# Kernel tuning notes

Measured on AMD Instinct MI355X. Metric: run time of the kernel, lower is better.

Reference implementation:

```python
import jax, jax.numpy as jnp
import numpy as np

UNITS = 768
OUT_STEPS = 64
INPUT_DIM = 96


def setup_inputs() -> dict:
    key = jax.random.key(0)
    ks = jax.random.split(key, 7)
    B, T = 2048, 24
    s_ih = 1.0 / np.sqrt(UNITS)
    inputs = jax.random.normal(ks[0], (B, T, INPUT_DIM), dtype=jnp.float32)
    # PyTorch LSTMCell params: weight_ih [4U, I], weight_hh [4U, U], biases [4U]
    W_ih = jax.random.uniform(ks[1], (4 * UNITS, INPUT_DIM), minval=-s_ih, maxval=s_ih, dtype=jnp.float32)
    W_hh = jax.random.uniform(ks[2], (4 * UNITS, UNITS), minval=-s_ih, maxval=s_ih, dtype=jnp.float32)
    b_ih = jax.random.uniform(ks[3], (4 * UNITS,), minval=-s_ih, maxval=s_ih, dtype=jnp.float32)
    b_hh = jax.random.uniform(ks[4], (4 * UNITS,), minval=-s_ih, maxval=s_ih, dtype=jnp.float32)
    # Dense: Linear(units, input_dim)
    s_d = 1.0 / np.sqrt(UNITS)
    W_d = jax.random.uniform(ks[5], (INPUT_DIM, UNITS), minval=-s_d, maxval=s_d, dtype=jnp.float32)
    b_d = jax.random.uniform(ks[6], (INPUT_DIM,), minval=-s_d, maxval=s_d, dtype=jnp.float32)
    return {"inputs": inputs, "W_ih": W_ih, "W_hh": W_hh, "b_ih": b_ih, "b_hh": b_hh, "W_d": W_d, "b_d": b_d}


def _lstm_cell(x, h, c, W_ih, W_hh, b_ih, b_hh):
    # gates: [B, 4U], PyTorch gate order i, f, g, o
    gates = x @ W_ih.T + b_ih + h @ W_hh.T + b_hh
    i, f, g, o = jnp.split(gates, 4, axis=-1)
    i = jax.nn.sigmoid(i)
    f = jax.nn.sigmoid(f)
    g = jnp.tanh(g)
    o = jax.nn.sigmoid(o)
    c_new = f * c + i * g
    h_new = o * jnp.tanh(c_new)
    return h_new, c_new


def reference(inputs, W_ih, W_hh, b_ih, b_hh, W_d, b_d):
    B = inputs.shape[0]
    h0 = jnp.zeros((B, UNITS), dtype=inputs.dtype)
    c0 = jnp.zeros((B, UNITS), dtype=inputs.dtype)
    # warmup: feed last timestep
    x0 = inputs[:, -1, :]
    h, c = _lstm_cell(x0, h0, c0, W_ih, W_hh, b_ih, b_hh)
    pred0 = h @ W_d.T + b_d

    def step(carry, _):
        pred, h, c = carry
        h2, c2 = _lstm_cell(pred, h, c, W_ih, W_hh, b_ih, b_hh)
        pred2 = h2 @ W_d.T + b_d
        return (pred2, h2, c2), pred2

    _, preds_rest = jax.lax.scan(step, (pred0, h, c), None, length=OUT_STEPS - 1)
    # preds_rest: [out_steps-1, B, I] -> stack with pred0 along time axis 1
    preds = jnp.concatenate([pred0[None], preds_rest], axis=0)  # [out_steps, B, I]
    return jnp.transpose(preds, (1, 0, 2))  # [B, out_steps, I]
```

## Files before the change

kernel.cpp:

```cpp
#include <hip/hip_runtime.h>
#include <hip/hip_bf16.h>
#include <stdint.h>

typedef __hip_bfloat16 bf16_t;
typedef __attribute__((ext_vector_type(4))) float f32x4;
typedef __attribute__((ext_vector_type(8))) short s16x8;

#define UNITS 768
#define NCOLS 3072
#define NPRED 96
#define MROWS 2048
#define BM 128
#define BN 128
#define BK 32

#define WAIT_VMCNT8 0xF78

#define GLL16(ldsp, gp) \
  __builtin_amdgcn_global_load_lds((const __attribute__((address_space(1))) void*)(gp), \
                                   (__attribute__((address_space(3))) void*)(ldsp), 16, 0, 0)

__device__ __forceinline__ float sigf(float x) {
    return __builtin_amdgcn_rcpf(1.f + __expf(-x));
}
__device__ __forceinline__ float tanh_fast(float x) {
    return 1.f - 2.f * __builtin_amdgcn_rcpf(1.f + __expf(2.f * x));
}


__global__ void prep_b0(const float* __restrict__ W_ih, bf16_t* __restrict__ B0T) {
    int idx = blockIdx.x * 256 + threadIdx.x;
    if (idx >= NCOLS * 96) return;
    int c = idx / 96, k = idx % 96;
    int u = ((c >> 6) << 4) + (c & 15);
    int g = (c >> 4) & 3;
    B0T[idx] = (bf16_t)W_ih[(g * UNITS + u) * 96 + k];
}

__global__ void prep_x0(const float* __restrict__ inputs, bf16_t* __restrict__ x0) {
    int idx = blockIdx.x * 256 + threadIdx.x;
    int b = idx / 96, k = idx % 96;
    x0[idx] = (bf16_t)inputs[(b * 24 + 23) * 96 + k];
}

__global__ void prep_bias(const float* __restrict__ b_ih, const float* __restrict__ b_hh,
                          const float* __restrict__ W_ih, const float* __restrict__ b_d,
                          float* __restrict__ b0_r, float* __restrict__ beff_r) {
    int c = blockIdx.x * 256 + threadIdx.x;
    if (c >= NCOLS) return;
    int u = ((c >> 6) << 4) + (c & 15);
    int g = (c >> 4) & 3;
    int r = g * UNITS + u;
    float v = b_ih[r] + b_hh[r];
    float acc = 0.f;
    for (int j = 0; j < 96; ++j) acc += W_ih[r * 96 + j] * b_d[j];
    b0_r[c] = v;
    beff_r[c] = v + acc;
}

__global__ void prep_beff2(const float* __restrict__ W_hh, const float* __restrict__ W_ih,
                           const float* __restrict__ W_d, bf16_t* __restrict__ BeffT) {
    __shared__ float sWih[64][96];
    __shared__ float sWd[96][64];
    const int c0 = blockIdx.x * 64, k0 = blockIdx.y * 64;
    const int tid = threadIdx.x;
    for (int i = tid; i < 64 * 96; i += 256) {
        int cc = i / 96, j = i % 96;
        int c = c0 + cc;
        int u = ((c >> 6) << 4) + (c & 15);
        int g = (c >> 4) & 3;
        sWih[cc][j] = W_ih[(g * UNITS + u) * 96 + j];
    }
    for (int i = tid; i < 96 * 64; i += 256) {
        int j = i / 64, kk = i % 64;
        sWd[j][kk] = W_d[j * UNITS + k0 + kk];
    }
    __syncthreads();
    const int kk = tid & 63;
    const int cc0 = (tid >> 6) * 16;
    for (int cc = cc0; cc < cc0 + 16; ++cc) {
        float acc = 0.f;
#pragma unroll 12
        for (int j = 0; j < 96; ++j) acc += sWih[cc][j] * sWd[j][kk];
        int c = c0 + cc;
        int u = ((c >> 6) << 4) + (c & 15);
        int g = (c >> 4) & 3;
        int r = g * UNITS + u;
        BeffT[(size_t)c * UNITS + k0 + kk] = (bf16_t)(W_hh[(size_t)r * UNITS + k0 + kk] + acc);
    }
}

__global__ void prep_wdt(const float* __restrict__ W_d, bf16_t* __restrict__ BeffT) {
    int idx = blockIdx.x * 256 + threadIdx.x;
    int c = idx / UNITS, k = idx % UNITS;
    float v = (c < NPRED) ? W_d[c * UNITS + k] : 0.f;
    BeffT[(size_t)(NCOLS + c) * UNITS + k] = (bf16_t)v;
}

__global__ __launch_bounds__(256, 2)
void step_kernel(const bf16_t* __restrict__ A,
                 const bf16_t* __restrict__ BT,
                 const float* __restrict__ bias_r,
                 const float* __restrict__ b_d,
                 float* __restrict__ c_state,
                 bf16_t* __restrict__ h_out,
                 float* __restrict__ out,
                 int Kdim, int nt_off, int t, int is_first)
{
    __shared__ bf16_t sAll[4][2][BM * BK];

    const int tid = threadIdx.x;
    const int wave = tid >> 6;
    const int lane = tid & 63;
    const int wr = wave >> 1, wc = wave & 1;
    const int l15 = lane & 15, l4 = lane >> 4;

    const int per = gridDim.x >> 3;
    const int g = (blockIdx.x & 7) * per + (blockIdx.x >> 3);
    const int nt = nt_off + (g >> 4);
    const int mt = g & 15;
    const int m0 = mt * BM;
    const int n0 = nt * BN;
    const bool is_pred = (nt >= 24);

    const int u = nt * 32 + wc * 16 + l15;
    const int slot = nt * 16 + mt;
    float* cbase = c_state + (((size_t)slot * 4 + wave) * 64 + lane) * 16;
    f32x4 cold4[4];
    float bi[4];
#pragma unroll
    for (int q = 0; q < 4; ++q) cold4[q] = f32x4{0.f, 0.f, 0.f, 0.f};
    if (!is_pred) {
        if (!is_first) {
#pragma unroll
            for (int q = 0; q < 4; ++q) cold4[q] = *(const f32x4*)(cbase + q * 4);
        }
#pragma unroll
        for (int f = 0; f < 4; ++f) bi[f] = bias_r[n0 + wc * 64 + f * 16 + l15];
    } else {
#pragma unroll
        for (int f = 0; f < 4; ++f) {
            int j = wc * 64 + f * 16 + l15;
            bi[f] = (j < NPRED) ? b_d[j] : 0.f;
        }
    }
    asm volatile("" ::: "memory");

    f32x4 acc[4][4];
#pragma unroll
    for (int i = 0; i < 4; ++i)
#pragma unroll
        for (int j = 0; j < 4; ++j) acc[i][j] = f32x4{0.f, 0.f, 0.f, 0.f};

    const int o0 = wave * 1024 + lane * 16;
    const int nk = Kdim >> 5;

#define STAGE(BUF, KT) do {                                                         \
        const int _kt = ((KT) < nk) ? (KT) : (nk - 1);                              \
        const int _k0 = _kt << 5;                                                   \
        bf16_t* _dA = &sAll[(BUF)][0][0];                                           \
        bf16_t* _dB = &sAll[(BUF)][1][0];                                           \
        _Pragma("unroll")                                                           \
        for (int _r = 0; _r < 2; ++_r) {                                            \
            int _ob = o0 + _r * 4096;                                               \
            int _row = _ob >> 6;                                                    \
            int _kb = _ob & 63;                                                     \
            const bf16_t* _gA = A + (size_t)(m0 + _row) * Kdim + _k0 + (_kb >> 1);  \
            GLL16(_dA + ((wave * 1024 + _r * 4096) >> 1), _gA);                     \
            const bf16_t* _gB = BT + (size_t)(n0 + _row) * Kdim + _k0 + (_kb >> 1); \
            GLL16(_dB + ((wave * 1024 + _r * 4096) >> 1), _gB);                     \
        }                                                                           \
    } while (0)

    STAGE(0, 0);
    STAGE(1, 1);
    STAGE(2, 2);

    for (int kt = 0; kt < nk; ++kt) {
        __builtin_amdgcn_s_waitcnt(WAIT_VMCNT8);
        __builtin_amdgcn_s_barrier();
        asm volatile("" ::: "memory");

        const int cb = kt & 3;
        const char* sAc = (const char*)&sAll[cb][0][0];
        const char* sBc = (const char*)&sAll[cb][1][0];

        s16x8 af[4], bfr[4];
#pragma unroll
        for (int f = 0; f < 4; ++f) {
            af[f]  = *(const s16x8*)(sAc + (wr * 64 + f * 16 + l15) * 64 + l4 * 16);
            bfr[f] = *(const s16x8*)(sBc + (wc * 64 + f * 16 + l15) * 64 + l4 * 16);
        }

        STAGE((kt + 3) & 3, kt + 3);

#pragma unroll
        for (int i = 0; i < 4; ++i)
#pragma unroll
            for (int j = 0; j < 4; ++j)
                acc[i][j] = __builtin_amdgcn_mfma_f32_16x16x32_bf16(af[i], bfr[j], acc[i][j], 0, 0, 0);
    }
#undef STAGE

    if (!is_pred) {
        f32x4 cnew4[4];
#pragma unroll
        for (int i = 0; i < 4; ++i) {
#pragma unroll
            for (int r = 0; r < 4; ++r) {
                int row = m0 + wr * 64 + i * 16 + l4 * 4 + r;
                float gi = acc[i][0][r] + bi[0];
                float gf = acc[i][1][r] + bi[1];
                float gg = acc[i][2][r] + bi[2];
                float go = acc[i][3][r] + bi[3];
                float si = sigf(gi);
                float sf = sigf(gf);
                float tg = tanh_fast(gg);
                float so = sigf(go);
                float cn = sf * cold4[i][r] + si * tg;
                cnew4[i][r] = cn;
                h_out[(size_t)row * UNITS + u] = (bf16_t)(so * tanh_fast(cn));
            }
        }
#pragma unroll
        for (int q = 0; q < 4; ++q) *(f32x4*)(cbase + q * 4) = cnew4[q];
    } else {
#pragma unroll
        for (int f = 0; f < 4; ++f) {
            int j = wc * 64 + f * 16 + l15;
            if (j < NPRED) {
#pragma unroll
                for (int i = 0; i < 4; ++i)
#pragma unroll
                    for (int r = 0; r < 4; ++r) {
                        int row = m0 + wr * 64 + i * 16 + l4 * 4 + r;
                        out[((size_t)row * 64 + (t - 1)) * NPRED + j] = acc[i][f][r] + bi[f];
                    }
            }
        }
    }
}

extern "C" void kernel_launch(void* const* d_in, const int* in_sizes, int n_in,
                              void* d_out, int out_size, void* d_ws, size_t ws_size,
                              hipStream_t stream)
{
    const float* inputs = (const float*)d_in[0];
    const float* W_ih   = (const float*)d_in[1];
    const float* W_hh   = (const float*)d_in[2];
    const float* b_ih   = (const float*)d_in[3];
    const float* b_hh   = (const float*)d_in[4];
    const float* W_d    = (const float*)d_in[5];
    const float* b_d    = (const float*)d_in[6];
    float* out = (float*)d_out;

    char* ws = (char*)d_ws;
    size_t off = 0;
    auto alloc = [&](size_t bytes) -> char* {
        char* p = ws + off;
        off = (off + bytes + 255) & ~(size_t)255;
        return p;
    };
    bf16_t* B0T   = (bf16_t*)alloc((size_t)NCOLS * 96 * 2);
    bf16_t* BeffT = (bf16_t*)alloc((size_t)3200 * UNITS * 2);
    bf16_t* x0    = (bf16_t*)alloc((size_t)MROWS * 96 * 2);
    bf16_t* h0    = (bf16_t*)alloc((size_t)MROWS * UNITS * 2);
    bf16_t* h1    = (bf16_t*)alloc((size_t)MROWS * UNITS * 2);
    float*  cst   = (float*)alloc((size_t)MROWS * UNITS * 4);
    float*  b0r   = (float*)alloc(NCOLS * 4);
    float*  beffr = (float*)alloc(NCOLS * 4);

    prep_b0   <<<(NCOLS * 96 + 255) / 256, 256, 0, stream>>>(W_ih, B0T);
    prep_x0   <<<(MROWS * 96) / 256, 256, 0, stream>>>(inputs, x0);
    prep_bias <<<(NCOLS + 255) / 256, 256, 0, stream>>>(b_ih, b_hh, W_ih, b_d, b0r, beffr);
    prep_beff2<<<dim3(48, 12), 256, 0, stream>>>(W_hh, W_ih, W_d, BeffT);
    prep_wdt  <<<(128 * UNITS) / 256, 256, 0, stream>>>(W_d, BeffT);

    bf16_t* h[2] = {h0, h1};

    step_kernel<<<384, 256, 0, stream>>>(x0, B0T, b0r, b_d, cst, h[1], out, 96, 0, 0, 1);
    for (int n = 1; n < 64; ++n)
        step_kernel<<<400, 256, 0, stream>>>(h[n & 1], BeffT, beffr, b_d, cst,
                                             h[(n + 1) & 1], out, UNITS, 0, n, 0);
    step_kernel<<<16, 256, 0, stream>>>(h[0], BeffT, beffr, b_d, cst, h[1], out,
                                        UNITS, 24, 64, 0);
    (void)ws_size; (void)in_sizes; (void)n_in; (void)out_size;
}
```

Baseline: 1.407 ms.

## Pre-swizzle operands into MFMA fragment layout and load directly to registers

Weights and the hidden state are rearranged into a fragment-major layout, so each lane's 16-byte MFMA operand sits contiguously in global memory. The step kernel then drops LDS staging and barriers and loads A/B fragments straight into registers, using a 3-deep register ring. The LSTM epilogue writes h in the same swizzled layout so the next step can read it directly. This removes LDS traffic and block-wide synchronisation. In exchange it costs more VGPRs, loses the sharing of tiles across waves, so each wave fetches its own operands through L1/L2, and adds prep passes.

New measurement: 1.349 ms. 4.1% less time.

```diff
diff --git a/kernel.cpp b/kernel.cpp
--- a/kernel.cpp
+++ b/kernel.cpp
@@ -10,15 +10,6 @@
 #define NCOLS 3072
 #define NPRED 96
 #define MROWS 2048
-#define BM 128
-#define BN 128
-#define BK 32
-
-#define WAIT_VMCNT8 0xF78
-
-#define GLL16(ldsp, gp) \
-  __builtin_amdgcn_global_load_lds((const __attribute__((address_space(1))) void*)(gp), \
-                                   (__attribute__((address_space(3))) void*)(ldsp), 16, 0, 0)
 
 __device__ __forceinline__ float sigf(float x) {
     return __builtin_amdgcn_rcpf(1.f + __expf(-x));
@@ -39,8 +30,14 @@
 
 __global__ void prep_x0(const float* __restrict__ inputs, bf16_t* __restrict__ x0) {
     int idx = blockIdx.x * 256 + threadIdx.x;
-    int b = idx / 96, k = idx % 96;
-    x0[idx] = (bf16_t)inputs[(b * 24 + 23) * 96 + k];
+    int j = idx & 7;
+    int l = (idx >> 3) & 63;
+    int fg = idx >> 9;
+    int kf = fg % 3;
+    int mf = fg / 3;
+    int m = mf * 16 + (l & 15);
+    int k = kf * 32 + (l >> 4) * 8 + j;
+    x0[idx] = (bf16_t)inputs[(m * 24 + 23) * 96 + k];
 }
 
 __global__ void prep_bias(const float* __restrict__ b_ih, const float* __restrict__ b_hh,
@@ -97,18 +94,32 @@
     BeffT[(size_t)(NCOLS + c) * UNITS + k] = (bf16_t)v;
 }
 
+__global__ void prep_swz(const bf16_t* __restrict__ src, bf16_t* __restrict__ dst,
+                         int Knk, int K, int total) {
+    int idx = blockIdx.x * 256 + threadIdx.x;
+    if (idx >= total) return;
+    int j = idx & 7;
+    int l = (idx >> 3) & 63;
+    int fg = idx >> 9;
+    int f = fg & 3;
+    int rest = fg >> 2;
+    int kf = rest % Knk;
+    int nw = rest / Knk;
+    int c = (nw >> 1) * 128 + (nw & 1) * 64 + f * 16 + (l & 15);
+    int k = kf * 32 + (l >> 4) * 8 + j;
+    dst[idx] = src[(size_t)c * K + k];
+}
+
 __global__ __launch_bounds__(256, 2)
 void step_kernel(const bf16_t* __restrict__ A,
-                 const bf16_t* __restrict__ BT,
+                 const bf16_t* __restrict__ B,
                  const float* __restrict__ bias_r,
                  const float* __restrict__ b_d,
                  float* __restrict__ c_state,
                  bf16_t* __restrict__ h_out,
                  float* __restrict__ out,
-                 int Kdim, int nt_off, int t, int is_first)
+                 int Knk, int nt_off, int t, int is_first)
 {
-    __shared__ bf16_t sAll[4][2][BM * BK];
-
     const int tid = threadIdx.x;
     const int wave = tid >> 6;
     const int lane = tid & 63;
@@ -119,9 +130,17 @@
     const int g = (blockIdx.x & 7) * per + (blockIdx.x >> 3);
     const int nt = nt_off + (g >> 4);
     const int mt = g & 15;
-    const int m0 = mt * BM;
-    const int n0 = nt * BN;
+    const int n0 = nt * 128;
     const bool is_pred = (nt >= 24);
+
+    const bf16_t* Ab[4];
+#pragma unroll
+    for (int i = 0; i < 4; ++i)
+        Ab[i] = A + ((size_t)((mt * 8 + wr * 4 + i) * Knk) * 64 + lane) * 8;
+    const bf16_t* Bb[4];
+#pragma unroll
+    for (int f = 0; f < 4; ++f)
+        Bb[f] = B + ((size_t)((nt * 2 + wc) * Knk * 4 + f) * 64 + lane) * 8;
 
     const int u = nt * 32 + wc * 16 + l15;
     const int slot = nt * 16 + mt;
@@ -144,7 +163,6 @@
             bi[f] = (j < NPRED) ? b_d[j] : 0.f;
         }
     }
-    asm volatile("" ::: "memory");
 
     f32x4 acc[4][4];
 #pragma unroll
@@ -152,63 +170,51 @@
 #pragma unroll
         for (int j = 0; j < 4; ++j) acc[i][j] = f32x4{0.f, 0.f, 0.f, 0.f};
 
-    const int o0 = wave * 1024 + lane * 16;
-    const int nk = Kdim >> 5;
-
-#define STAGE(BUF, KT) do {                                                         \
-        const int _kt = ((KT) < nk) ? (KT) : (nk - 1);                              \
-        const int _k0 = _kt << 5;                                                   \
-        bf16_t* _dA = &sAll[(BUF)][0][0];                                           \
-        bf16_t* _dB = &sAll[(BUF)][1][0];                                           \
-        _Pragma("unroll")                                                           \
-        for (int _r = 0; _r < 2; ++_r) {                                            \
-            int _ob = o0 + _r * 4096;                                               \
-            int _row = _ob >> 6;                                                    \
-            int _kb = _ob & 63;                                                     \
-            const bf16_t* _gA = A + (size_t)(m0 + _row) * Kdim + _k0 + (_kb >> 1);  \
-            GLL16(_dA + ((wave * 1024 + _r * 4096) >> 1), _gA);                     \
-            const bf16_t* _gB = BT + (size_t)(n0 + _row) * Kdim + _k0 + (_kb >> 1); \
-            GLL16(_dB + ((wave * 1024 + _r * 4096) >> 1), _gB);                     \
-        }                                                                           \
+    s16x8 afr[3][4], bfr[3][4];
+    const int nk = Knk;
+
+#define LOADK(BUF, KT) do {                                                          \
+        _Pragma("unroll")                                                            \
+        for (int _i = 0; _i < 4; ++_i)                                               \
+            afr[BUF][_i] = *(const s16x8*)(Ab[_i] + (size_t)(KT) * 512);             \
+        _Pragma("unroll")                                                            \
+        for (int _f = 0; _f < 4; ++_f)                                               \
+            bfr[BUF][_f] = *(const s16x8*)(Bb[_f] + (size_t)(KT) * 2048);            \
     } while (0)
-
-    STAGE(0, 0);
-    STAGE(1, 1);
-    STAGE(2, 2);
-
-    for (int kt = 0; kt < nk; ++kt) {
-        __builtin_amdgcn_s_waitcnt(WAIT_VMCNT8);
-        __builtin_amdgcn_s_barrier();
-        asm volatile("" ::: "memory");
-
-        const int cb = kt & 3;
-        const char* sAc = (const char*)&sAll[cb][0][0];
-        const char* sBc = (const char*)&sAll[cb][1][0];
-
-        s16x8 af[4], bfr[4];
-#pragma unroll
-        for (int f = 0; f < 4; ++f) {
-            af[f]  = *(const s16x8*)(sAc + (wr * 64 + f * 16 + l15) * 64 + l4 * 16);
-            bfr[f] = *(const s16x8*)(sBc + (wc * 64 + f * 16 + l15) * 64 + l4 * 16);
-        }
-
-        STAGE((kt + 3) & 3, kt + 3);
-
-#pragma unroll
-        for (int i = 0; i < 4; ++i)
-#pragma unroll
-            for (int j = 0; j < 4; ++j)
-                acc[i][j] = __builtin_amdgcn_mfma_f32_16x16x32_bf16(af[i], bfr[j], acc[i][j], 0, 0, 0);
-    }
-#undef STAGE
+#define MF(BUF) do {                                                                 \
+        _Pragma("unroll")                                                            \
+        for (int _i = 0; _i < 4; ++_i)                                               \
+            _Pragma("unroll")                                                        \
+            for (int _j = 0; _j < 4; ++_j)                                           \
+                acc[_i][_j] = __builtin_amdgcn_mfma_f32_16x16x32_bf16(               \
+                    afr[BUF][_i], bfr[BUF][_j], acc[_i][_j], 0, 0, 0);               \
+    } while (0)
+
+    LOADK(0, 0);
+    LOADK(1, 1);
+    const int nk3 = nk / 3;
+    for (int b3 = 0; b3 < nk3; ++b3) {
+        const int kt = b3 * 3;
+        if (kt + 2 < nk) LOADK(2, kt + 2);
+        MF(0);
+        if (kt + 3 < nk) LOADK(0, kt + 3);
+        MF(1);
+        if (kt + 4 < nk) LOADK(1, kt + 4);
+        MF(2);
+    }
+#undef LOADK
+#undef MF
 
     if (!is_pred) {
+        const int kq = wc * 2 + (l15 >> 3);
+        const int jj = l15 & 7;
         f32x4 cnew4[4];
 #pragma unroll
         for (int i = 0; i < 4; ++i) {
+            const int mf = mt * 8 + wr * 4 + i;
+            bf16_t* hb = h_out + (size_t)(mf * 24 + nt) * 512;
 #pragma unroll
             for (int r = 0; r < 4; ++r) {
-                int row = m0 + wr * 64 + i * 16 + l4 * 4 + r;
                 float gi = acc[i][0][r] + bi[0];
                 float gf = acc[i][1][r] + bi[1];
                 float gg = acc[i][2][r] + bi[2];
@@ -219,7 +225,8 @@
                 float so = sigf(go);
                 float cn = sf * cold4[i][r] + si * tg;
                 cnew4[i][r] = cn;
-                h_out[(size_t)row * UNITS + u] = (bf16_t)(so * tanh_fast(cn));
+                int lp = (l4 * 4 + r) | (kq << 4);
+                hb[lp * 8 + jj] = (bf16_t)(so * tanh_fast(cn));
             }
         }
 #pragma unroll
@@ -233,7 +240,7 @@
                 for (int i = 0; i < 4; ++i)
 #pragma unroll
                     for (int r = 0; r < 4; ++r) {
-                        int row = m0 + wr * 64 + i * 16 + l4 * 4 + r;
+                        int row = mt * 128 + wr * 64 + i * 16 + l4 * 4 + r;
                         out[((size_t)row * 64 + (t - 1)) * NPRED + j] = acc[i][f][r] + bi[f];
                     }
             }
@@ -262,27 +269,31 @@
         return p;
     };
     bf16_t* B0T   = (bf16_t*)alloc((size_t)NCOLS * 96 * 2);
+    bf16_t* B0s   = (bf16_t*)alloc((size_t)NCOLS * 96 * 2);
     bf16_t* BeffT = (bf16_t*)alloc((size_t)3200 * UNITS * 2);
-    bf16_t* x0    = (bf16_t*)alloc((size_t)MROWS * 96 * 2);
+    bf16_t* Bs    = (bf16_t*)alloc((size_t)3200 * UNITS * 2);
+    bf16_t* x0s   = (bf16_t*)alloc((size_t)MROWS * 96 * 2);
     bf16_t* h0    = (bf16_t*)alloc((size_t)MROWS * UNITS * 2);
     bf16_t* h1    = (bf16_t*)alloc((size_t)MROWS * UNITS * 2);
-    float*  cst   = (float*)alloc((size_t)MROWS * UNITS * 4);
+    float*  cst   = (float*)alloc((size_t)384 * 4 * 64 * 16 * 4);
     float*  b0r   = (float*)alloc(NCOLS * 4);
     float*  beffr = (float*)alloc(NCOLS * 4);
 
     prep_b0   <<<(NCOLS * 96 + 255) / 256, 256, 0, stream>>>(W_ih, B0T);
-    prep_x0   <<<(MROWS * 96) / 256, 256, 0, stream>>>(inputs, x0);
+    prep_swz  <<<(NCOLS * 96 + 255) / 256, 256, 0, stream>>>(B0T, B0s, 3, 96, NCOLS * 96);
+    prep_x0   <<<(MROWS * 96) / 256, 256, 0, stream>>>(inputs, x0s);
     prep_bias <<<(NCOLS + 255) / 256, 256, 0, stream>>>(b_ih, b_hh, W_ih, b_d, b0r, beffr);
     prep_beff2<<<dim3(48, 12), 256, 0, stream>>>(W_hh, W_ih, W_d, BeffT);
     prep_wdt  <<<(128 * UNITS) / 256, 256, 0, stream>>>(W_d, BeffT);
+    prep_swz  <<<(3200 * UNITS + 255) / 256, 256, 0, stream>>>(BeffT, Bs, 24, UNITS, 3200 * UNITS);
 
     bf16_t* h[2] = {h0, h1};
 
-    step_kernel<<<384, 256, 0, stream>>>(x0, B0T, b0r, b_d, cst, h[1], out, 96, 0, 0, 1);
+    step_kernel<<<384, 256, 0, stream>>>(x0s, B0s, b0r, b_d, cst, h[1], out, 3, 0, 0, 1);
     for (int n = 1; n < 64; ++n)
-        step_kernel<<<400, 256, 0, stream>>>(h[n & 1], BeffT, beffr, b_d, cst,
-                                             h[(n + 1) & 1], out, UNITS, 0, n, 0);
-    step_kernel<<<16, 256, 0, stream>>>(h[0], BeffT, beffr, b_d, cst, h[1], out,
-                                        UNITS, 24, 64, 0);
+        step_kernel<<<400, 256, 0, stream>>>(h[n & 1], Bs, beffr, b_d, cst,
+                                             h[(n + 1) & 1], out, 24, 0, n, 0);
+    step_kernel<<<16, 256, 0, stream>>>(h[0], Bs, beffr, b_d, cst, h[1], out,
+                                        24, 24, 64, 0);
     (void)ws_size; (void)in_sizes; (void)n_in; (void)out_size;
 }
```
